# Kernel tuning notes

Measured on AMD Instinct MI355X. Metric: run time of the kernel, lower is better.

Reference implementation:

```python
import jax, jax.numpy as jnp
import numpy as np

B, CIN, H, W = 16, 32, 256, 256
COUT, KH, KW = 32, 3, 3
NUM_EXPERTS = 8
PAD = ((1, 1), (1, 1))  # static 'same' padding for 3x3, stride 1, dilation 1


def setup_inputs() -> dict:
    key = jax.random.key(0)
    k_x, k_r, k_w, k_b = jax.random.split(key, 4)
    x = jax.random.normal(k_x, (B, CIN, H, W), dtype=jnp.float32)
    # routing weights are typically sigmoid/softmax outputs in [0,1]
    routing_weights = jax.nn.softmax(jax.random.normal(k_r, (B, NUM_EXPERTS), dtype=jnp.float32), axis=-1)
    num_params = COUT * CIN * KH * KW  # groups=1 -> in_channels//groups = CIN
    expert_weight = jax.random.normal(k_w, (NUM_EXPERTS, num_params), dtype=jnp.float32) * 0.05
    expert_bias = jax.random.normal(k_b, (NUM_EXPERTS, COUT), dtype=jnp.float32) * 0.05
    return {"x": x, "routing_weights": routing_weights,
            "expert_weight": expert_weight, "expert_bias": expert_bias}


def reference(x, routing_weights, expert_weight, expert_bias):
    b = x.shape[0]
    # Per-sample kernels: [B, num_params] -> [B, COUT, CIN, KH, KW]
    w = jnp.matmul(routing_weights, expert_weight).reshape(b, COUT, CIN, KH, KW)
    bias = jnp.matmul(routing_weights, expert_bias)  # [B, COUT]

    def conv_one(xi, wi):
        # xi: [CIN, H, W], wi: [COUT, CIN, KH, KW]
        return jax.lax.conv_general_dilated(
            xi[None], wi, window_strides=(1, 1), padding=PAD,
            dimension_numbers=("NCHW", "OIHW", "NCHW"))[0]

    out = jax.vmap(conv_one)(x, w)  # [B, COUT, H, W]
    out = out + bias[:, :, None, None]
    return out
```

## Files before the change

### kernel.cpp

```cpp
#include <hip/hip_runtime.h>

#define B_   16
#define CIN  32
#define COUT 32
#define HH   256
#define WW   256
#define NE   8
#define NTAP 9
#define KTOT (NTAP * CIN)

#define TH 8
#define TW 32
#define LROWS (TH + 2)
#define LCOLS (TW + 2)
#define PXS   40

typedef __attribute__((ext_vector_type(8))) short  short8;
typedef __attribute__((ext_vector_type(4))) float  floatx4;

__device__ __forceinline__ unsigned short f2bf(float f) {
    unsigned int u = __float_as_uint(f);
    u += 0x7FFFu + ((u >> 16) & 1u);
    return (unsigned short)(u >> 16);
}

__global__ __launch_bounds__(256) void prep_weights(
    const float* __restrict__ routing,
    const float* __restrict__ ew,
    const float* __restrict__ eb,
    unsigned short* __restrict__ ws_w,
    float* __restrict__ ws_b)
{
    const int b = blockIdx.x;
    const int t = threadIdx.x;
    float r[NE];
#pragma unroll
    for (int e = 0; e < NE; ++e) r[e] = routing[b * NE + e];

    for (int idx = t; idx < COUT * KTOT; idx += 256) {
        const int co  = idx / KTOT;
        const int k   = idx - co * KTOT;
        const int tap = k >> 5;
        const int ci  = k & 31;
        float acc = 0.f;
#pragma unroll
        for (int e = 0; e < NE; ++e)
            acc += r[e] * ew[e * (COUT * CIN * 9) + co * (CIN * 9) + ci * 9 + tap];
        ws_w[(b * COUT + co) * KTOT + k] = f2bf(acc);
    }
    if (t < COUT) {
        float acc = 0.f;
#pragma unroll
        for (int e = 0; e < NE; ++e) acc += r[e] * eb[e * COUT + t];
        ws_b[b * COUT + t] = acc;
    }
}

__global__ __launch_bounds__(256, 4) void condconv_mfma(
    const float* __restrict__ x,
    const unsigned short* __restrict__ wsw,
    const float* __restrict__ wsb,
    float* __restrict__ out)
{
    __shared__ __align__(16) unsigned short s_x[LROWS * LCOLS * PXS];

    const int b    = blockIdx.z;
    const int x0   = blockIdx.x * TW;
    const int y0   = blockIdx.y * TH;
    const int t    = threadIdx.x;
    const int lane = t & 63;
    const int wv   = t >> 6;
    const int ln   = lane & 15;
    const int quad = lane >> 4;

    for (int task = t; task < LROWS * LCOLS * 4; task += 256) {
        const int p   = task >> 2;
        const int c   = task & 3;
        const int row = p / LCOLS;
        const int col = p - row * LCOLS;
        const int gy  = y0 + row - 1;
        const int gx  = x0 + col - 1;
        short8 pk;
        if (gy >= 0 && gy < HH && gx >= 0 && gx < WW) {
            const float* src = x + (((size_t)b * CIN + c * 8) * HH + gy) * WW + gx;
#pragma unroll
            for (int u = 0; u < 8; ++u)
                pk[u] = (short)f2bf(src[(size_t)u * HH * WW]);
        } else {
#pragma unroll
            for (int u = 0; u < 8; ++u) pk[u] = 0;
        }
        *(short8*)&s_x[p * PXS + c * 8] = pk;
    }

    const unsigned short* wb = wsw + (size_t)b * COUT * KTOT;
    short8 afc0 = *(const short8*)(wb + ln * KTOT + quad * 8);
    short8 afc1 = *(const short8*)(wb + (16 + ln) * KTOT + quad * 8);

    floatx4 acc[4][2];
#pragma unroll
    for (int tt = 0; tt < 4; ++tt)
#pragma unroll
        for (int h = 0; h < 2; ++h)
            acc[tt][h] = (floatx4){0.f, 0.f, 0.f, 0.f};

    int base[4];
#pragma unroll
    for (int tt = 0; tt < 4; ++tt)
        base[tt] = ((2 * wv + (tt >> 1)) * LCOLS + (tt & 1) * 16 + ln) * PXS + quad * 8;

    __syncthreads();

#pragma unroll 1
    for (int tap = 0; tap < NTAP; ++tap) {
        const int tn = (tap < NTAP - 1) ? tap + 1 : NTAP - 1;
        const short8 afn0 = *(const short8*)(wb + ln * KTOT + tn * 32 + quad * 8);
        const short8 afn1 = *(const short8*)(wb + (16 + ln) * KTOT + tn * 32 + quad * 8);
        const int dy  = tap / 3;
        const int dx  = tap - dy * 3;
        const int off = (dy * LCOLS + dx) * PXS;
#pragma unroll
        for (int tt = 0; tt < 4; ++tt) {
            const short8 bfr = *(const short8*)&s_x[base[tt] + off];
            acc[tt][0] = __builtin_amdgcn_mfma_f32_16x16x32_bf16(afc0, bfr, acc[tt][0], 0, 0, 0);
            acc[tt][1] = __builtin_amdgcn_mfma_f32_16x16x32_bf16(afc1, bfr, acc[tt][1], 0, 0, 0);
        }
        afc0 = afn0;
        afc1 = afn1;
    }

    float bias_v[2][4];
#pragma unroll
    for (int h = 0; h < 2; ++h)
#pragma unroll
        for (int rg = 0; rg < 4; ++rg)
            bias_v[h][rg] = wsb[b * COUT + h * 16 + quad * 4 + rg];

#pragma unroll
    for (int tt = 0; tt < 4; ++tt) {
        const int r  = 2 * wv + (tt >> 1);
        const int q  = tt & 1;
        const int gy = y0 + r;
        const int gx = x0 + q * 16 + ln;
#pragma unroll
        for (int h = 0; h < 2; ++h)
#pragma unroll
            for (int rg = 0; rg < 4; ++rg) {
                const int co = h * 16 + quad * 4 + rg;
                out[(((size_t)b * COUT + co) * HH + gy) * WW + gx] = acc[tt][h][rg] + bias_v[h][rg];
            }
    }
}

extern "C" void kernel_launch(void* const* d_in, const int* in_sizes, int n_in,
                              void* d_out, int out_size, void* d_ws, size_t ws_size,
                              hipStream_t stream) {
    const float* x       = (const float*)d_in[0];
    const float* routing = (const float*)d_in[1];
    const float* ew      = (const float*)d_in[2];
    const float* eb      = (const float*)d_in[3];
    float* out = (float*)d_out;

    unsigned short* ws_w = (unsigned short*)d_ws;
    float* ws_b = (float*)((char*)d_ws + (size_t)B_ * COUT * KTOT * 2);

    prep_weights<<<dim3(B_), dim3(256), 0, stream>>>(routing, ew, eb, ws_w, ws_b);

    dim3 grid(WW / TW, HH / TH, B_);
    condconv_mfma<<<grid, dim3(256), 0, stream>>>(x, ws_w, ws_b, out);
}
```

Baseline: 299.4 us.

## Widen conv tile to 64 columns and load input with float4 vectors

Doubles the output tile width so each wave computes eight 16-pixel MFMA tiles instead of four, which cuts halo overhead and amortizes per-block weight loads over more pixels. The shared-memory fill now reads aligned float4 chunks per channel row instead of scalar loads, then converts to bf16 and scatters into the channel-interleaved tile. In exchange the kernel uses more registers and more LDS per block, so occupancy hint drops to 3 blocks per CU, and the aligned loads fetch some unused edge columns.

```diff
diff --git a/kernel.cpp b/kernel.cpp
--- a/kernel.cpp
+++ b/kernel.cpp
@@ -10,10 +10,11 @@
 #define KTOT (NTAP * CIN)
 
 #define TH 8
-#define TW 32
+#define TW 64
 #define LROWS (TH + 2)
 #define LCOLS (TW + 2)
 #define PXS   40
+#define NI    ((TW + 8) / 4)
 
 typedef __attribute__((ext_vector_type(8))) short  short8;
 typedef __attribute__((ext_vector_type(4))) float  floatx4;
@@ -56,7 +57,7 @@
     }
 }
 
-__global__ __launch_bounds__(256, 4) void condconv_mfma(
+__global__ __launch_bounds__(256, 3) void condconv_mfma(
     const float* __restrict__ x,
     const unsigned short* __restrict__ wsw,
     const float* __restrict__ wsb,
@@ -73,41 +74,50 @@
     const int ln   = lane & 15;
     const int quad = lane >> 4;
 
-    for (int task = t; task < LROWS * LCOLS * 4; task += 256) {
-        const int p   = task >> 2;
-        const int c   = task & 3;
-        const int row = p / LCOLS;
-        const int col = p - row * LCOLS;
+    for (int task = t; task < LROWS * NI * 4; task += 256) {
+        const int cg  = task & 3;
+        const int ri  = task >> 2;
+        const int i   = ri % NI;
+        const int row = ri / NI;
         const int gy  = y0 + row - 1;
-        const int gx  = x0 + col - 1;
-        short8 pk;
+        const int gx  = x0 + 4 * i - 4;
+        floatx4 v[8];
         if (gy >= 0 && gy < HH && gx >= 0 && gx < WW) {
-            const float* src = x + (((size_t)b * CIN + c * 8) * HH + gy) * WW + gx;
+            const float* src = x + (((size_t)b * CIN + cg * 8) * HH + gy) * WW + gx;
 #pragma unroll
             for (int u = 0; u < 8; ++u)
-                pk[u] = (short)f2bf(src[(size_t)u * HH * WW]);
+                v[u] = *(const floatx4*)(src + (size_t)u * HH * WW);
         } else {
 #pragma unroll
-            for (int u = 0; u < 8; ++u) pk[u] = 0;
+            for (int u = 0; u < 8; ++u) v[u] = (floatx4){0.f, 0.f, 0.f, 0.f};
         }
-        *(short8*)&s_x[p * PXS + c * 8] = pk;
+#pragma unroll
+        for (int j = 0; j < 4; ++j) {
+            const int lcol = 4 * i + j - 3;
+            if (lcol >= 0 && lcol < LCOLS) {
+                short8 pk;
+#pragma unroll
+                for (int u = 0; u < 8; ++u) pk[u] = (short)f2bf(v[u][j]);
+                *(short8*)&s_x[(row * LCOLS + lcol) * PXS + cg * 8] = pk;
+            }
+        }
     }
 
     const unsigned short* wb = wsw + (size_t)b * COUT * KTOT;
     short8 afc0 = *(const short8*)(wb + ln * KTOT + quad * 8);
     short8 afc1 = *(const short8*)(wb + (16 + ln) * KTOT + quad * 8);
 
-    floatx4 acc[4][2];
+    floatx4 acc[8][2];
 #pragma unroll
-    for (int tt = 0; tt < 4; ++tt)
+    for (int tt = 0; tt < 8; ++tt)
 #pragma unroll
         for (int h = 0; h < 2; ++h)
             acc[tt][h] = (floatx4){0.f, 0.f, 0.f, 0.f};
 
-    int base[4];
+    int base[8];
 #pragma unroll
-    for (int tt = 0; tt < 4; ++tt)
-        base[tt] = ((2 * wv + (tt >> 1)) * LCOLS + (tt & 1) * 16 + ln) * PXS + quad * 8;
+    for (int tt = 0; tt < 8; ++tt)
+        base[tt] = ((2 * wv + (tt >> 2)) * LCOLS + (tt & 3) * 16 + ln) * PXS + quad * 8;
 
     __syncthreads();
 
@@ -120,7 +130,7 @@
         const int dx  = tap - dy * 3;
         const int off = (dy * LCOLS + dx) * PXS;
 #pragma unroll
-        for (int tt = 0; tt < 4; ++tt) {
+        for (int tt = 0; tt < 8; ++tt) {
             const short8 bfr = *(const short8*)&s_x[base[tt] + off];
             acc[tt][0] = __builtin_amdgcn_mfma_f32_16x16x32_bf16(afc0, bfr, acc[tt][0], 0, 0, 0);
             acc[tt][1] = __builtin_amdgcn_mfma_f32_16x16x32_bf16(afc1, bfr, acc[tt][1], 0, 0, 0);
@@ -137,9 +147,9 @@
             bias_v[h][rg] = wsb[b * COUT + h * 16 + quad * 4 + rg];
 
 #pragma unroll
-    for (int tt = 0; tt < 4; ++tt) {
-        const int r  = 2 * wv + (tt >> 1);
-        const int q  = tt & 1;
+    for (int tt = 0; tt < 8; ++tt) {
+        const int r  = 2 * wv + (tt >> 2);
+        const int q  = tt & 3;
         const int gy = y0 + r;
         const int gx = x0 + q * 16 + ln;
 #pragma unroll
```

Measured after the change: 287.2 us. 1.04x faster.
